# Performance work log

Hardware: AMD Instinct MI355X
Metric: run time of the kernel (lower is better)

The kernel has to match this reference:

```python
import jax, jax.numpy as jnp
import numpy as np

N, E, G, IN, H, L, C = 20000, 320000, 128, 16, 64, 4, 10
AVG_D_LOG = float(np.log(17.0))  # log(avg_degree + 1)


def setup_inputs() -> dict:
    key = jax.random.key(0)
    ks = jax.random.split(key, 24)
    p = lambda k, shape: jax.random.normal(k, shape, dtype=jnp.float32) * 0.05
    return dict(
        h=jax.random.normal(ks[0], (N, IN), jnp.float32),
        snorm_n=jax.random.uniform(ks[1], (N, 1), jnp.float32, 0.05, 1.0),
        embW=p(ks[2], (IN, H)), embB=p(ks[3], (H,)),
        preW=p(ks[4], (L, 2 * H, H)), preB=p(ks[5], (L, H)),
        postW=p(ks[6], (L, 13 * H, H)), postB=p(ks[7], (L, H)),
        mixW=p(ks[8], (L, H, H)), mixB=p(ks[9], (L, H)),
        r1W=p(ks[10], (H, H // 2)), r1B=p(ks[11], (H // 2,)),
        r2W=p(ks[12], (H // 2, H // 4)), r2B=p(ks[13], (H // 4,)),
        r3W=p(ks[14], (H // 4, C)), r3B=p(ks[15], (C,)),
        src=jax.random.randint(ks[16], (E,), 0, N),
        dst=jax.random.randint(ks[17], (E,), 0, N),
        graph_ids=jnp.sort(jax.random.randint(ks[18], (N,), 0, G)),
    )


def _pna_forward(h, snorm_n, embW, embB, preW, preB, postW, postB, mixW, mixB,
                 r1W, r1B, r2W, r2B, r3W, r3B, src, dst, graph_ids):
    # Degree-based scalers (computed once; graph is fixed across layers)
    deg = jax.ops.segment_sum(jnp.ones((E,), h.dtype), dst, num_segments=N)  # [N]
    degc = jnp.maximum(deg, 1.0)[:, None]
    logd = jnp.log(deg + 1.0)
    amp = (logd / AVG_D_LOG)[:, None]                      # amplification scaler
    att = (AVG_D_LOG / jnp.maximum(logd, 1e-5))[:, None]   # attenuation scaler
    has_nb = (deg > 0.0)[:, None]

    x = h @ embW + embB  # node embedding [N, H]
    for i in range(L):
        x_in = x
        # pretrans: per-edge message from cat(h_src, h_dst)  [E, H]
        m = jnp.concatenate([x[src], x[dst]], axis=-1) @ preW[i] + preB[i]
        # multi-aggregator reduce at dst: mean, max, min, std
        mean = jax.ops.segment_sum(m, dst, num_segments=N) / degc
        msq = jax.ops.segment_sum(m * m, dst, num_segments=N) / degc
        std = jnp.sqrt(jax.nn.relu(msq - mean * mean) + 1e-5)
        mx = jnp.where(has_nb, jax.ops.segment_max(m, dst, num_segments=N), 0.0)
        mn = jnp.where(has_nb, jax.ops.segment_min(m, dst, num_segments=N), 0.0)
        agg = jnp.concatenate([mean, mx, mn, std], axis=-1)  # [N, 4H]
        # degree scalers: identity, amplification, attenuation -> [N, 12H]
        scaled = jnp.concatenate([agg, agg * amp, agg * att], axis=-1)
        # posttrans over cat(scaled_agg, h) -> [N, H]
        y = jnp.concatenate([scaled, x], axis=-1) @ postW[i] + postB[i]
        # tower mixing network (LeakyReLU FC)
        y = jax.nn.leaky_relu(y @ mixW[i] + mixB[i])
        y = y * snorm_n          # graph norm
        x = x_in + y             # residual
    # mean-nodes readout per graph
    gsum = jax.ops.segment_sum(x, graph_ids, num_segments=G)
    cnt = jnp.maximum(jax.ops.segment_sum(jnp.ones((N,), x.dtype), graph_ids, num_segments=G), 1.0)
    hg = gsum / cnt[:, None]
    # MLPReadout: two halving ReLU layers + classifier
    hg = jax.nn.relu(hg @ r1W + r1B)
    hg = jax.nn.relu(hg @ r2W + r2B)
    return hg @ r3W + r3B  # [G, C]


def reference(h, snorm_n, embW, embB, preW, preB, postW, postB, mixW, mixB,
              r1W, r1B, r2W, r2B, r3W, r3B, src, dst, graph_ids):
    return _pna_forward(h, snorm_n, embW, embB, preW, preB, postW, postB,
                        mixW, mixB, r1W, r1B, r2W, r2B, r3W, r3B,
                        src, dst, graph_ids)
```

## Files before the change

kernel.cpp:

```cpp
#include <hip/hip_runtime.h>
#include <math.h>

#define N_ 20000
#define E_ 320000
#define G_ 128
#define IN_ 16
#define H_ 64
#define L_ 4
#define C_ 10
#define AVG_D_LOG 2.8332133440562162f

union F4 { float4 v; float f[4]; };

typedef _Float16 h8 __attribute__((ext_vector_type(8)));
typedef _Float16 h4 __attribute__((ext_vector_type(4)));
typedef float f4x __attribute__((ext_vector_type(4)));
#define MFMA16(a, b, c) __builtin_amdgcn_mfma_f32_16x16x32_f16((a), (b), (c), 0, 0, 0)


__global__ __launch_bounds__(256) void k_setup(
    const float* __restrict__ h, const float* __restrict__ embW, const float* __restrict__ embB,
    float* __restrict__ x,
    const float* __restrict__ preW, const float* __restrict__ postW, const float* __restrict__ mixW,
    _Float16* __restrict__ preWT, _Float16* __restrict__ postWT, _Float16* __restrict__ mixWT,
    const int* __restrict__ dst, int* __restrict__ deg) {
  __shared__ float tl[64][68];
  int bb = blockIdx.x, tid = threadIdx.x;
  if (bb < 5000) {
    int n = bb * 4 + (tid >> 6);
    int c = tid & 63;
    float acc = embB[c];
#pragma unroll
    for (int k = 0; k < IN_; k++) acc += h[n * IN_ + k] * embW[k * H_ + c];
    x[n * H_ + c] = acc;
  } else if (bb < 5052) {
    int t = bb - 5000;
    int l = t / 13, kt = t % 13, k0 = kt * 64;
    const float* Wsrc = postW + (size_t)l * 53248;
    _Float16* Wdst = postWT + (size_t)l * 53248;
    int r = tid >> 4, q4 = (tid & 15) * 4;
#pragma unroll
    for (int p = 0; p < 4; p++) {
      int rr = p * 16 + r;
      float4 v = *(const float4*)(Wsrc + (size_t)(k0 + rr) * 64 + q4);
      tl[rr][q4 + 0] = v.x; tl[rr][q4 + 1] = v.y;
      tl[rr][q4 + 2] = v.z; tl[rr][q4 + 3] = v.w;
    }
    __syncthreads();
#pragma unroll
    for (int p = 0; p < 4; p++) {
      int o = p * 256 + tid;
      int c = o >> 4, j4 = (o & 15) * 4;
      h4 hv;
      hv[0] = (_Float16)tl[j4 + 0][c]; hv[1] = (_Float16)tl[j4 + 1][c];
      hv[2] = (_Float16)tl[j4 + 2][c]; hv[3] = (_Float16)tl[j4 + 3][c];
      *(h4*)(Wdst + (size_t)c * 832 + k0 + j4) = hv;
    }
  } else if (bb < 5244) {
    int idx = (bb - 5052) * 256 + tid;
    if (idx < 32768) {
      int l = idx >> 13, r = idx & 8191;
      int c = r >> 6, k = r & 63;
      preWT[idx] = (_Float16)preW[l * 8192 + k * 64 + c];
    } else {
      int j = idx - 32768;
      int l = j >> 12, r = j & 4095;
      int c = r >> 6, k = r & 63;
      mixWT[j] = (_Float16)mixW[l * 4096 + k * 64 + c];
    }
  } else {
    int e = (bb - 5244) * 256 + tid;
    if (e < E_) atomicAdd(&deg[dst[e]], 1);
  }
}


__global__ __launch_bounds__(1024) void k_scan(
    const int* __restrict__ deg, int* __restrict__ offs,
    float* __restrict__ ampv, float* __restrict__ attv,
    float* __restrict__ invd, float* __restrict__ hnb,
    const float* __restrict__ x, const _Float16* __restrict__ preWT,
    const float* __restrict__ preB, _Float16* __restrict__ ah, float* __restrict__ b) {
  int bx = blockIdx.x, tid = threadIdx.x;
  if (bx == 0) {
    __shared__ int sh[1024];
    int t = tid;
    int base = t * 20;
    int local[20];
    int s = 0;
    if (t < 1000) {
#pragma unroll
      for (int c = 0; c < 5; c++) {
        int4 v = *(const int4*)(deg + base + c * 4);
        local[c * 4 + 0] = s; s += v.x;
        local[c * 4 + 1] = s; s += v.y;
        local[c * 4 + 2] = s; s += v.z;
        local[c * 4 + 3] = s; s += v.w;
      }
    }
    sh[t] = s;
    __syncthreads();
    for (int off = 1; off < 1024; off <<= 1) {
      int v = (t >= off) ? sh[t - off] : 0;
      __syncthreads();
      sh[t] += v;
      __syncthreads();
    }
    if (t < 1000) {
      int excl = sh[t] - s;
#pragma unroll
      for (int c = 0; c < 5; c++) {
        int4 o;
        o.x = excl + local[c * 4 + 0];
        o.y = excl + local[c * 4 + 1];
        o.z = excl + local[c * 4 + 2];
        o.w = excl + local[c * 4 + 3];
        *(int4*)(offs + base + c * 4) = o;
      }
    }
    if (t == 0) offs[N_] = sh[1023];
  } else if (bx < 21) {
    int idx = (bx - 1) * 1024 + tid;
    if (idx < N_) {
      float d = (float)deg[idx];
      float logd = logf(d + 1.f);
      ampv[idx] = logd / AVG_D_LOG;
      attv[idx] = AVG_D_LOG / fmaxf(logd, 1e-5f);
      invd[idx] = 1.f / fmaxf(d, 1.f);
      hnb[idx] = d > 0.f ? 1.f : 0.f;
    }
  } else {
    int sub = tid >> 8;
    int t2 = tid & 255;
    int n0 = (bx - 21) * 128 + sub * 32;
    if (n0 >= N_) return;
    int lane = t2 & 63, wv = t2 >> 6;
    int mt = wv & 1, nh = wv >> 1;
    int l15 = lane & 15, k0q = (lane >> 4) * 8;
    int mrow = n0 + mt * 16 + l15;
    const float* xr = x + (size_t)mrow * 64;
    const _Float16* wb0 = preWT + (size_t)(nh * 64 + l15) * 64 + k0q;
    f4x acc0 = {0.f,0.f,0.f,0.f}, acc1 = {0.f,0.f,0.f,0.f}, acc2 = {0.f,0.f,0.f,0.f}, acc3 = {0.f,0.f,0.f,0.f};
#pragma unroll
    for (int kb = 0; kb < 64; kb += 32) {
      int ko = kb + k0q;
      F4 xa, xb2;
      xa.v = *(const float4*)(xr + ko);
      xb2.v = *(const float4*)(xr + ko + 4);
      h8 af;
      af[0]=(_Float16)xa.f[0]; af[1]=(_Float16)xa.f[1]; af[2]=(_Float16)xa.f[2]; af[3]=(_Float16)xa.f[3];
      af[4]=(_Float16)xb2.f[0]; af[5]=(_Float16)xb2.f[1]; af[6]=(_Float16)xb2.f[2]; af[7]=(_Float16)xb2.f[3];
      acc0 = MFMA16(af, *(const h8*)(wb0 + kb), acc0);
      acc1 = MFMA16(af, *(const h8*)(wb0 + 1024 + kb), acc1);
      acc2 = MFMA16(af, *(const h8*)(wb0 + 2048 + kb), acc2);
      acc3 = MFMA16(af, *(const h8*)(wb0 + 3072 + kb), acc3);
    }
    int rbase = n0 + mt * 16 + (lane >> 4) * 4;
    f4x accs[4] = {acc0, acc1, acc2, acc3};
#pragma unroll
    for (int t = 0; t < 4; t++) {
      int col = nh * 64 + t * 16 + l15;
#pragma unroll
      for (int r = 0; r < 4; r++) {
        int n = rbase + r;
        if (col < 64) ah[(size_t)n * 64 + col] = (_Float16)accs[t][r];
        else          b[(size_t)n * 64 + (col - 64)] = accs[t][r] + preB[col - 64];
      }
    }
  }
}


__global__ __launch_bounds__(256) void k_scatter(
    const int* __restrict__ src, const int* __restrict__ dst,
    const int* __restrict__ offs, int* __restrict__ cursor, int* __restrict__ csr) {
  int e = blockIdx.x * 256 + threadIdx.x;
  if (e < E_) {
    int d = dst[e];
    int pos = offs[d] + atomicAdd(&cursor[d], 1);
    csr[pos] = src[e];
  }
}


__global__ __launch_bounds__(256, 5) void k_layer(
    const _Float16* __restrict__ ahin, const float* __restrict__ bin,
    const int* __restrict__ offs, const int* __restrict__ csr,
    const float* __restrict__ invd, const float* __restrict__ hnb,
    const _Float16* __restrict__ WT, const float* __restrict__ Bv,
    const _Float16* __restrict__ mixWT, const float* __restrict__ mixB,
    const float* __restrict__ ampv, const float* __restrict__ attv,
    const float* __restrict__ snorm, float* __restrict__ x,
    const _Float16* __restrict__ preWT, const float* __restrict__ preB,
    _Float16* __restrict__ ahout, float* __restrict__ bout, int do_pre) {
  __shared__ _Float16 aggs[16 * 280];
  __shared__ _Float16 ys[16 * 88];
  __shared__ _Float16 xs[16 * 88];
  __shared__ _Float16 xt[16 * 88];
  __shared__ float xs32[16 * 68];
  __shared__ int csr_s[1024];
  __shared__ int soffs[17];
  __shared__ float scal[48];
  int tid = threadIdx.x;
  int n0 = blockIdx.x * 16;
  int lane = tid & 63, wv = tid >> 6;

  int e0 = offs[n0];
  int ecnt = offs[n0 + 16] - e0;
  {
    int row = tid >> 4, qq = tid & 15;
    F4 xv; xv.v = *(const float4*)(x + (size_t)(n0 + row) * 64 + qq * 4);
    h4 xh;
    xh[0] = (_Float16)xv.f[0]; xh[1] = (_Float16)xv.f[1];
    xh[2] = (_Float16)xv.f[2]; xh[3] = (_Float16)xv.f[3];
    *(h4*)(xt + row * 88 + qq * 4) = xh;
    *(float4*)(xs32 + row * 68 + qq * 4) = xv.v;
  }
  if (tid < 17) soffs[tid] = offs[n0 + tid];
  if (tid >= 32 && tid < 48) {
    int i = tid - 32;
    scal[i] = ampv[n0 + i];
    scal[16 + i] = attv[n0 + i];
    scal[32 + i] = snorm[n0 + i];
  }
  int nlA = tid >> 4, qA = tid & 15;
  F4 bv; bv.v = *(const float4*)(bin + (size_t)(n0 + nlA) * 64 + qA * 4);
  float inv = invd[n0 + nlA], hn = hnb[n0 + nlA];
  int col0 = wv * 16 + (tid & 15);
  float b0v = Bv[col0];
  float mb0 = mixB[col0];
  {
    int cnt = ecnt < 1024 ? ecnt : 1024;
    for (int i = tid; i < cnt; i += 256) csr_s[i] = csr[e0 + i];
  }
  __syncthreads();

  {
    int nl = nlA, q = qA;
    int o0 = soffs[nl];
    int deg = soffs[nl + 1] - o0;
    float sum[4], sq[4], mx[4], mn[4];
#pragma unroll
    for (int i = 0; i < 4; i++) {
      sum[i] = 0.f; sq[i] = 0.f;
      mx[i] = -__builtin_inff(); mn[i] = __builtin_inff();
    }
#define GLD_(S) (*(const h4*)(ahin + (size_t)(S) * 64 + q * 4))
#define PROC1_(AV)                                                       \
    do {                                                                 \
      _Pragma("unroll")                                                  \
      for (int i = 0; i < 4; i++) {                                      \
        float v0 = (float)AV[i];                                         \
        sum[i] += v0; sq[i] += v0 * v0;                                  \
        mx[i] = fmaxf(mx[i], v0); mn[i] = fminf(mn[i], v0);              \
      }                                                                  \
    } while (0)
    if (ecnt <= 1024) {
      int lo = o0 - e0;
      int j = 0;
      h4 A0, A1, A2, A3;
      if (j + 3 < deg) {
        A0 = GLD_(csr_s[lo]);     A1 = GLD_(csr_s[lo + 1]);
        A2 = GLD_(csr_s[lo + 2]); A3 = GLD_(csr_s[lo + 3]);
      }
      for (; j + 7 < deg; j += 4) {
        int s0 = csr_s[lo + j + 4], s1 = csr_s[lo + j + 5];
        int s2 = csr_s[lo + j + 6], s3 = csr_s[lo + j + 7];
        h4 B0 = GLD_(s0), B1 = GLD_(s1), B2 = GLD_(s2), B3 = GLD_(s3);
        PROC1_(A0); PROC1_(A1); PROC1_(A2); PROC1_(A3);
        A0 = B0; A1 = B1; A2 = B2; A3 = B3;
      }
      if (j + 3 < deg) { PROC1_(A0); PROC1_(A1); PROC1_(A2); PROC1_(A3); j += 4; }
      for (; j < deg; j++) { h4 a0 = GLD_(csr_s[lo + j]); PROC1_(a0); }
    } else {
      int j = 0;
      for (; j < deg; j++) { h4 a0 = GLD_(csr[o0 + j]); PROC1_(a0); }
    }
#undef GLD_
#undef PROC1_
    h4 hm, hx, hmn, hs;
#pragma unroll
    for (int i = 0; i < 4; i++) {
      float mean_a = sum[i] * inv;
      float var = sq[i] * inv - mean_a * mean_a;
      hs[i] = (_Float16)sqrtf(fmaxf(var, 0.f) + 1e-5f);
      bool nb = hn > 0.5f;
      hm[i] = (_Float16)(nb ? (mean_a + bv.f[i]) : 0.f);
      hx[i] = (_Float16)(nb ? (mx[i] + bv.f[i]) : 0.f);
      hmn[i] = (_Float16)(nb ? (mn[i] + bv.f[i]) : 0.f);
    }
    _Float16* ap = aggs + nl * 280 + q * 4;
    *(h4*)(ap) = hm;
    *(h4*)(ap + 64) = hx;
    *(h4*)(ap + 128) = hmn;
    *(h4*)(ap + 192) = hs;
  }
  __syncthreads();

  int l15 = lane & 15, k0q = (lane >> 4) * 8;
  const _Float16* ag = aggs + (size_t)l15 * 280 + k0q;
  const _Float16* w0 = WT + (size_t)col0 * 832 + k0q;
  f4x aI = {0.f,0.f,0.f,0.f}, aA = {0.f,0.f,0.f,0.f}, aT = {0.f,0.f,0.f,0.f};
#pragma unroll 4
  for (int kb = 0; kb < 256; kb += 32) {
    h8 af = *(const h8*)(ag + kb);
    aI = MFMA16(af, *(const h8*)(w0 + kb), aI);
    aA = MFMA16(af, *(const h8*)(w0 + 256 + kb), aA);
    aT = MFMA16(af, *(const h8*)(w0 + 512 + kb), aT);
  }
  const _Float16* xtr = xt + (size_t)l15 * 88 + k0q;
#pragma unroll
  for (int kb = 0; kb < 64; kb += 32) {
    h8 af = *(const h8*)(xtr + kb);
    aI = MFMA16(af, *(const h8*)(w0 + 768 + kb), aI);
  }
  int qr = (lane >> 4) * 4;
  int rbase = n0 + qr;
#pragma unroll
  for (int r = 0; r < 4; r++) {
    float amp = scal[qr + r], att = scal[16 + qr + r];
    ys[(qr + r) * 88 + col0] = (_Float16)(aI[r] + b0v + amp * aA[r] + att * aT[r]);
  }
  __syncthreads();
  f4x m0 = {0.f,0.f,0.f,0.f};
  const _Float16* yr = ys + (size_t)l15 * 88 + k0q;
  const _Float16* mw0 = mixWT + (size_t)col0 * 64 + k0q;
#pragma unroll
  for (int kb = 0; kb < 64; kb += 32) {
    h8 af = *(const h8*)(yr + kb);
    m0 = MFMA16(af, *(const h8*)(mw0 + kb), m0);
  }
#pragma unroll
  for (int r = 0; r < 4; r++) {
    int n = rbase + r;
    float sn = scal[32 + qr + r];
    float t0 = m0[r] + mb0; t0 = t0 > 0.f ? t0 : 0.01f * t0;
    float xo0 = xs32[(qr + r) * 68 + col0] + t0 * sn;
    x[(size_t)n * 64 + col0] = xo0;
    xs[(qr + r) * 88 + col0] = (_Float16)xo0;
  }

  if (do_pre) {
    __syncthreads();
    int ch = wv;
    const _Float16* xf = xs + (size_t)l15 * 88 + k0q;
    const _Float16* wb0 = preWT + (size_t)(ch * 32 + l15) * 64 + k0q;
    f4x p0 = {0.f,0.f,0.f,0.f}, p1 = {0.f,0.f,0.f,0.f};
#pragma unroll
    for (int kb = 0; kb < 64; kb += 32) {
      h8 af = *(const h8*)(xf + kb);
      p0 = MFMA16(af, *(const h8*)(wb0 + kb), p0);
      p1 = MFMA16(af, *(const h8*)(wb0 + 1024 + kb), p1);
    }
    int prb = n0 + (lane >> 4) * 4;
    f4x accs[2] = {p0, p1};
#pragma unroll
    for (int t = 0; t < 2; t++) {
      int col = ch * 32 + t * 16 + l15;
#pragma unroll
      for (int r = 0; r < 4; r++) {
        int n = prb + r;
        if (col < 64) ahout[(size_t)n * 64 + col] = (_Float16)accs[t][r];
        else          bout[(size_t)n * 64 + (col - 64)] = accs[t][r] + preB[col - 64];
      }
    }
  }
}


__device__ inline int lower_bound_gid(const int* __restrict__ gid, int val) {
  int lo = 0, hi = N_;
  while (lo < hi) {
    int mid = (lo + hi) >> 1;
    if (gid[mid] < val) lo = mid + 1; else hi = mid;
  }
  return lo;
}

__global__ __launch_bounds__(512) void k_readout_fused(
    const float* __restrict__ x, const int* __restrict__ gid,
    const float* __restrict__ r1W, const float* __restrict__ r1B,
    const float* __restrict__ r2W, const float* __restrict__ r2B,
    const float* __restrict__ r3W, const float* __restrict__ r3B,
    float* __restrict__ out) {
  __shared__ float part[8 * 64];
  __shared__ float hg[64];
  __shared__ float t1[32];
  __shared__ float t2[16];
  int g = blockIdx.x, tid = threadIdx.x;
  int lo = lower_bound_gid(gid, g);
  int hi = lower_bound_gid(gid, g + 1);
  int c = tid & 63, w = tid >> 6;
  float s = 0.f;
  for (int n = lo + w; n < hi; n += 8) s += x[(size_t)n * 64 + c];
  part[w * 64 + c] = s;
  __syncthreads();
  if (w == 0) {
    float tot = 0.f;
#pragma unroll
    for (int p = 0; p < 8; p++) tot += part[p * 64 + c];
    float cnt = (float)(hi - lo);
    if (cnt < 1.f) cnt = 1.f;
    hg[c] = tot / cnt;
  }
  __syncthreads();
  if (tid < 32) {
    float acc = r1B[tid];
#pragma unroll 8
    for (int k = 0; k < 64; k++) acc += hg[k] * r1W[k * 32 + tid];
    t1[tid] = fmaxf(acc, 0.f);
  }
  __syncthreads();
  if (tid < 16) {
    float acc = r2B[tid];
#pragma unroll 8
    for (int k = 0; k < 32; k++) acc += t1[k] * r2W[k * 16 + tid];
    t2[tid] = fmaxf(acc, 0.f);
  }
  __syncthreads();
  if (tid < 10) {
    float acc = r3B[tid];
#pragma unroll
    for (int k = 0; k < 16; k++) acc += t2[k] * r3W[k * 10 + tid];
    out[g * 10 + tid] = acc;
  }
}


extern "C" void kernel_launch(void* const* d_in, const int* in_sizes, int n_in,
                              void* d_out, int out_size, void* d_ws, size_t ws_size,
                              hipStream_t stream) {
  const float* h     = (const float*)d_in[0];
  const float* snorm = (const float*)d_in[1];
  const float* embW  = (const float*)d_in[2];
  const float* embB  = (const float*)d_in[3];
  const float* preW  = (const float*)d_in[4];
  const float* preB  = (const float*)d_in[5];
  const float* postW = (const float*)d_in[6];
  const float* postB = (const float*)d_in[7];
  const float* mixW  = (const float*)d_in[8];
  const float* mixB  = (const float*)d_in[9];
  const float* r1W   = (const float*)d_in[10];
  const float* r1B   = (const float*)d_in[11];
  const float* r2W   = (const float*)d_in[12];
  const float* r2B   = (const float*)d_in[13];
  const float* r3W   = (const float*)d_in[14];
  const float* r3B   = (const float*)d_in[15];
  const int* src     = (const int*)d_in[16];
  const int* dst     = (const int*)d_in[17];
  const int* gid     = (const int*)d_in[18];
  float* out = (float*)d_out;

  char* w = (char*)d_ws;
  float* x        = (float*)w; w += (size_t)N_ * 64 * 4;
  _Float16* ah0   = (_Float16*)w; w += (size_t)N_ * 64 * 2;
  _Float16* ah1   = (_Float16*)w; w += (size_t)N_ * 64 * 2;
  float* b0       = (float*)w; w += (size_t)N_ * 64 * 4;
  float* b1       = (float*)w; w += (size_t)N_ * 64 * 4;
  _Float16* preWT = (_Float16*)w; w += (size_t)4 * 128 * 64 * 2;
  _Float16* postWT= (_Float16*)w; w += (size_t)4 * 64 * 832 * 2;
  _Float16* mixWT = (_Float16*)w; w += (size_t)4 * 64 * 64 * 2;
  float* ampv = (float*)w; w += (size_t)N_ * 4;
  float* attv = (float*)w; w += (size_t)N_ * 4;
  float* invd = (float*)w; w += (size_t)N_ * 4;
  float* hnb  = (float*)w; w += (size_t)N_ * 4;
  int* csr    = (int*)w;   w += (size_t)E_ * 4;
  int* offs   = (int*)w;   w += (size_t)(N_ + 64) * 4;
  int* zbase  = (int*)w;
  int* deg    = (int*)w;   w += (size_t)N_ * 4;
  int* cursor = (int*)w;   w += (size_t)N_ * 4;

  hipMemsetAsync(zbase, 0, (size_t)2 * N_ * 4, stream);
  k_setup<<<6494, 256, 0, stream>>>(h, embW, embB, x, preW, postW, mixW,
                                    preWT, postWT, mixWT, dst, deg);
  k_scan<<<178, 1024, 0, stream>>>(deg, offs, ampv, attv, invd, hnb,
                                   x, preWT, preB, ah0, b0);
  k_scatter<<<1250, 256, 0, stream>>>(src, dst, offs, cursor, csr);
  int gb = N_ / 16;
  _Float16* ahs[2] = {ah0, ah1};
  float* bs[2] = {b0, b1};
  for (int l = 0; l < L_; l++) {
    int pin = l & 1, pout = 1 - pin;
    k_layer<<<gb, 256, 0, stream>>>(ahs[pin], bs[pin], offs, csr, invd, hnb,
                                    postWT + (size_t)l * 53248, postB + l * H_,
                                    mixWT + (size_t)l * 4096, mixB + l * H_,
                                    ampv, attv, snorm, x,
                                    preWT + (size_t)(l + 1 < L_ ? l + 1 : 0) * 8192,
                                    preB + (l + 1 < L_ ? l + 1 : 0) * H_,
                                    ahs[pout], bs[pout], l + 1 < L_ ? 1 : 0);
  }
  k_readout_fused<<<G_, 512, 0, stream>>>(x, gid, r1W, r1B, r2W, r2B, r3W, r3B, out);
}
```

Baseline: 268.7 us.

## Fuse per-layer launches into a persistent kernel with a grid barrier

Measured after the change: 911.2 us. 3.39x slower.

```diff
diff --git a/kernel.cpp b/kernel.cpp
--- a/kernel.cpp
+++ b/kernel.cpp
@@ -8,6 +8,7 @@
 #define H_ 64
 #define L_ 4
 #define C_ 10
+#define GB_ (N_ / 16)
 #define AVG_D_LOG 2.8332133440562162f
 
 union F4 { float4 v; float f[4]; };
@@ -183,38 +184,63 @@
 }
 
 
-__global__ __launch_bounds__(256, 5) void k_layer(
-    const _Float16* __restrict__ ahin, const float* __restrict__ bin,
+__device__ __forceinline__ void grid_bar(int* bar, int tid) {
+  __syncthreads();
+  if (tid == 0) {
+    __threadfence();
+    __hip_atomic_fetch_add(bar, 1, __ATOMIC_RELEASE, __HIP_MEMORY_SCOPE_AGENT);
+    long cnt = 0;
+    int v;
+    do {
+      v = __hip_atomic_load(bar, __ATOMIC_ACQUIRE, __HIP_MEMORY_SCOPE_AGENT);
+      if (v >= GB_) break;
+      __builtin_amdgcn_s_sleep(8);
+    } while (++cnt < (1L << 28));
+    __threadfence();
+  }
+  __syncthreads();
+}
+
+
+__global__ __launch_bounds__(256, 5) void k_layers(
+    const float* __restrict__ bin,
     const int* __restrict__ offs, const int* __restrict__ csr,
     const float* __restrict__ invd, const float* __restrict__ hnb,
-    const _Float16* __restrict__ WT, const float* __restrict__ Bv,
+    const _Float16* __restrict__ postWT, const float* __restrict__ postB,
     const _Float16* __restrict__ mixWT, const float* __restrict__ mixB,
     const float* __restrict__ ampv, const float* __restrict__ attv,
     const float* __restrict__ snorm, float* __restrict__ x,
     const _Float16* __restrict__ preWT, const float* __restrict__ preB,
-    _Float16* __restrict__ ahout, float* __restrict__ bout, int do_pre) {
+    _Float16* __restrict__ ah0g, _Float16* __restrict__ ah1g,
+    int* __restrict__ bar) {
   __shared__ _Float16 aggs[16 * 280];
   __shared__ _Float16 ys[16 * 88];
-  __shared__ _Float16 xs[16 * 88];
-  __shared__ _Float16 xt[16 * 88];
+  __shared__ _Float16 xtA[16 * 88];
+  __shared__ _Float16 xtB[16 * 88];
   __shared__ float xs32[16 * 68];
+  __shared__ float b_lds[16 * 68];
   __shared__ int csr_s[1024];
   __shared__ int soffs[17];
   __shared__ float scal[48];
   int tid = threadIdx.x;
   int n0 = blockIdx.x * 16;
   int lane = tid & 63, wv = tid >> 6;
+  int nlA = tid >> 4, qA = tid & 15;
+  int l15 = lane & 15, k0q = (lane >> 4) * 8;
+  int col0 = wv * 16 + l15;
+  int qr = (lane >> 4) * 4;
 
   int e0 = offs[n0];
   int ecnt = offs[n0 + 16] - e0;
   {
-    int row = tid >> 4, qq = tid & 15;
+    int row = nlA, qq = qA;
     F4 xv; xv.v = *(const float4*)(x + (size_t)(n0 + row) * 64 + qq * 4);
     h4 xh;
     xh[0] = (_Float16)xv.f[0]; xh[1] = (_Float16)xv.f[1];
     xh[2] = (_Float16)xv.f[2]; xh[3] = (_Float16)xv.f[3];
-    *(h4*)(xt + row * 88 + qq * 4) = xh;
+    *(h4*)(xtA + row * 88 + qq * 4) = xh;
     *(float4*)(xs32 + row * 68 + qq * 4) = xv.v;
+    *(float4*)(b_lds + row * 68 + qq * 4) = *(const float4*)(bin + (size_t)(n0 + row) * 64 + qq * 4);
   }
   if (tid < 17) soffs[tid] = offs[n0 + tid];
   if (tid >= 32 && tid < 48) {
@@ -223,146 +249,154 @@
     scal[16 + i] = attv[n0 + i];
     scal[32 + i] = snorm[n0 + i];
   }
-  int nlA = tid >> 4, qA = tid & 15;
-  F4 bv; bv.v = *(const float4*)(bin + (size_t)(n0 + nlA) * 64 + qA * 4);
   float inv = invd[n0 + nlA], hn = hnb[n0 + nlA];
-  int col0 = wv * 16 + (tid & 15);
-  float b0v = Bv[col0];
-  float mb0 = mixB[col0];
   {
     int cnt = ecnt < 1024 ? ecnt : 1024;
     for (int i = tid; i < cnt; i += 256) csr_s[i] = csr[e0 + i];
   }
   __syncthreads();
 
-  {
-    int nl = nlA, q = qA;
-    int o0 = soffs[nl];
-    int deg = soffs[nl + 1] - o0;
-    float sum[4], sq[4], mx[4], mn[4];
-#pragma unroll
-    for (int i = 0; i < 4; i++) {
-      sum[i] = 0.f; sq[i] = 0.f;
-      mx[i] = -__builtin_inff(); mn[i] = __builtin_inff();
-    }
-#define GLD_(S) (*(const h4*)(ahin + (size_t)(S) * 64 + q * 4))
+  for (int l = 0; l < L_; l++) {
+    const _Float16* ahin = (l & 1) ? ah1g : ah0g;
+    _Float16* ahout = (l & 1) ? ah0g : ah1g;
+    const _Float16* WT = postWT + (size_t)l * 53248;
+    const float* Bv = postB + l * H_;
+    const _Float16* mw = mixWT + (size_t)l * 4096;
+    const float* mB = mixB + l * H_;
+    _Float16* xt_cur = (l & 1) ? xtB : xtA;
+    _Float16* xt_nxt = (l & 1) ? xtA : xtB;
+
+    {
+      int o0 = soffs[nlA];
+      int deg = soffs[nlA + 1] - o0;
+      F4 bv; bv.v = *(const float4*)(b_lds + nlA * 68 + qA * 4);
+      float sum[4], sq[4], mx[4], mn[4];
+#pragma unroll
+      for (int i = 0; i < 4; i++) {
+        sum[i] = 0.f; sq[i] = 0.f;
+        mx[i] = -__builtin_inff(); mn[i] = __builtin_inff();
+      }
+#define GLD_(S) (*(const h4*)(ahin + (size_t)(S) * 64 + qA * 4))
 #define PROC1_(AV)                                                       \
-    do {                                                                 \
-      _Pragma("unroll")                                                  \
-      for (int i = 0; i < 4; i++) {                                      \
-        float v0 = (float)AV[i];                                         \
-        sum[i] += v0; sq[i] += v0 * v0;                                  \
-        mx[i] = fmaxf(mx[i], v0); mn[i] = fminf(mn[i], v0);              \
-      }                                                                  \
-    } while (0)
-    if (ecnt <= 1024) {
-      int lo = o0 - e0;
-      int j = 0;
-      h4 A0, A1, A2, A3;
-      if (j + 3 < deg) {
-        A0 = GLD_(csr_s[lo]);     A1 = GLD_(csr_s[lo + 1]);
-        A2 = GLD_(csr_s[lo + 2]); A3 = GLD_(csr_s[lo + 3]);
-      }
-      for (; j + 7 < deg; j += 4) {
-        int s0 = csr_s[lo + j + 4], s1 = csr_s[lo + j + 5];
-        int s2 = csr_s[lo + j + 6], s3 = csr_s[lo + j + 7];
-        h4 B0 = GLD_(s0), B1 = GLD_(s1), B2 = GLD_(s2), B3 = GLD_(s3);
-        PROC1_(A0); PROC1_(A1); PROC1_(A2); PROC1_(A3);
-        A0 = B0; A1 = B1; A2 = B2; A3 = B3;
-      }
-      if (j + 3 < deg) { PROC1_(A0); PROC1_(A1); PROC1_(A2); PROC1_(A3); j += 4; }
-      for (; j < deg; j++) { h4 a0 = GLD_(csr_s[lo + j]); PROC1_(a0); }
-    } else {
-      int j = 0;
-      for (; j < deg; j++) { h4 a0 = GLD_(csr[o0 + j]); PROC1_(a0); }
-    }
+      do {                                                               \
+        _Pragma("unroll")                                                \
+        for (int i = 0; i < 4; i++) {                                    \
+          float v0 = (float)AV[i];                                       \
+          sum[i] += v0; sq[i] += v0 * v0;                                \
+          mx[i] = fmaxf(mx[i], v0); mn[i] = fminf(mn[i], v0);            \
+        }                                                                \
+      } while (0)
+      if (ecnt <= 1024) {
+        int lo = o0 - e0;
+        int j = 0;
+        h4 A0, A1, A2, A3;
+        if (j + 3 < deg) {
+          A0 = GLD_(csr_s[lo]);     A1 = GLD_(csr_s[lo + 1]);
+          A2 = GLD_(csr_s[lo + 2]); A3 = GLD_(csr_s[lo + 3]);
+        }
+        for (; j + 7 < deg; j += 4) {
+          int s0 = csr_s[lo + j + 4], s1 = csr_s[lo + j + 5];
+          int s2 = csr_s[lo + j + 6], s3 = csr_s[lo + j + 7];
+          h4 B0 = GLD_(s0), B1 = GLD_(s1), B2 = GLD_(s2), B3 = GLD_(s3);
+          PROC1_(A0); PROC1_(A1); PROC1_(A2); PROC1_(A3);
+          A0 = B0; A1 = B1; A2 = B2; A3 = B3;
+        }
+        if (j + 3 < deg) { PROC1_(A0); PROC1_(A1); PROC1_(A2); PROC1_(A3); j += 4; }
+        for (; j < deg; j++) { h4 a0 = GLD_(csr_s[lo + j]); PROC1_(a0); }
+      } else {
+        for (int j = 0; j < deg; j++) { h4 a0 = GLD_(csr[o0 + j]); PROC1_(a0); }
+      }
 #undef GLD_
 #undef PROC1_
-    h4 hm, hx, hmn, hs;
-#pragma unroll
-    for (int i = 0; i < 4; i++) {
-      float mean_a = sum[i] * inv;
-      float var = sq[i] * inv - mean_a * mean_a;
-      hs[i] = (_Float16)sqrtf(fmaxf(var, 0.f) + 1e-5f);
-      bool nb = hn > 0.5f;
-      hm[i] = (_Float16)(nb ? (mean_a + bv.f[i]) : 0.f);
-      hx[i] = (_Float16)(nb ? (mx[i] + bv.f[i]) : 0.f);
-      hmn[i] = (_Float16)(nb ? (mn[i] + bv.f[i]) : 0.f);
-    }
-    _Float16* ap = aggs + nl * 280 + q * 4;
-    *(h4*)(ap) = hm;
-    *(h4*)(ap + 64) = hx;
-    *(h4*)(ap + 128) = hmn;
-    *(h4*)(ap + 192) = hs;
-  }
-  __syncthreads();
-
-  int l15 = lane & 15, k0q = (lane >> 4) * 8;
-  const _Float16* ag = aggs + (size_t)l15 * 280 + k0q;
-  const _Float16* w0 = WT + (size_t)col0 * 832 + k0q;
-  f4x aI = {0.f,0.f,0.f,0.f}, aA = {0.f,0.f,0.f,0.f}, aT = {0.f,0.f,0.f,0.f};
+      h4 hm, hx, hmn, hs;
+#pragma unroll
+      for (int i = 0; i < 4; i++) {
+        float mean_a = sum[i] * inv;
+        float var = sq[i] * inv - mean_a * mean_a;
+        hs[i] = (_Float16)sqrtf(fmaxf(var, 0.f) + 1e-5f);
+        bool nb = hn > 0.5f;
+        hm[i] = (_Float16)(nb ? (mean_a + bv.f[i]) : 0.f);
+        hx[i] = (_Float16)(nb ? (mx[i] + bv.f[i]) : 0.f);
+        hmn[i] = (_Float16)(nb ? (mn[i] + bv.f[i]) : 0.f);
+      }
+      _Float16* ap = aggs + nlA * 280 + qA * 4;
+      *(h4*)(ap) = hm;
+      *(h4*)(ap + 64) = hx;
+      *(h4*)(ap + 128) = hmn;
+      *(h4*)(ap + 192) = hs;
+    }
+    __syncthreads();
+
+    {
+      const _Float16* ag = aggs + (size_t)l15 * 280 + k0q;
+      const _Float16* w0 = WT + (size_t)col0 * 832 + k0q;
+      float b0v = Bv[col0];
+      float mb0 = mB[col0];
+      f4x aI = {0.f,0.f,0.f,0.f}, aA = {0.f,0.f,0.f,0.f}, aT = {0.f,0.f,0.f,0.f};
 #pragma unroll 4
-  for (int kb = 0; kb < 256; kb += 32) {
-    h8 af = *(const h8*)(ag + kb);
-    aI = MFMA16(af, *(const h8*)(w0 + kb), aI);
-    aA = MFMA16(af, *(const h8*)(w0 + 256 + kb), aA);
-    aT = MFMA16(af, *(const h8*)(w0 + 512 + kb), aT);
-  }
-  const _Float16* xtr = xt + (size_t)l15 * 88 + k0q;
-#pragma unroll
-  for (int kb = 0; kb < 64; kb += 32) {
-    h8 af = *(const h8*)(xtr + kb);
-    aI = MFMA16(af, *(const h8*)(w0 + 768 + kb), aI);
-  }
-  int qr = (lane >> 4) * 4;
-  int rbase = n0 + qr;
-#pragma unroll
-  for (int r = 0; r < 4; r++) {
-    float amp = scal[qr + r], att = scal[16 + qr + r];
-    ys[(qr + r) * 88 + col0] = (_Float16)(aI[r] + b0v + amp * aA[r] + att * aT[r]);
-  }
-  __syncthreads();
-  f4x m0 = {0.f,0.f,0.f,0.f};
-  const _Float16* yr = ys + (size_t)l15 * 88 + k0q;
-  const _Float16* mw0 = mixWT + (size_t)col0 * 64 + k0q;
-#pragma unroll
-  for (int kb = 0; kb < 64; kb += 32) {
-    h8 af = *(const h8*)(yr + kb);
-    m0 = MFMA16(af, *(const h8*)(mw0 + kb), m0);
-  }
-#pragma unroll
-  for (int r = 0; r < 4; r++) {
-    int n = rbase + r;
-    float sn = scal[32 + qr + r];
-    float t0 = m0[r] + mb0; t0 = t0 > 0.f ? t0 : 0.01f * t0;
-    float xo0 = xs32[(qr + r) * 68 + col0] + t0 * sn;
-    x[(size_t)n * 64 + col0] = xo0;
-    xs[(qr + r) * 88 + col0] = (_Float16)xo0;
-  }
-
-  if (do_pre) {
-    __syncthreads();
-    int ch = wv;
-    const _Float16* xf = xs + (size_t)l15 * 88 + k0q;
-    const _Float16* wb0 = preWT + (size_t)(ch * 32 + l15) * 64 + k0q;
-    f4x p0 = {0.f,0.f,0.f,0.f}, p1 = {0.f,0.f,0.f,0.f};
-#pragma unroll
-    for (int kb = 0; kb < 64; kb += 32) {
-      h8 af = *(const h8*)(xf + kb);
-      p0 = MFMA16(af, *(const h8*)(wb0 + kb), p0);
-      p1 = MFMA16(af, *(const h8*)(wb0 + 1024 + kb), p1);
-    }
-    int prb = n0 + (lane >> 4) * 4;
-    f4x accs[2] = {p0, p1};
-#pragma unroll
-    for (int t = 0; t < 2; t++) {
-      int col = ch * 32 + t * 16 + l15;
+      for (int kb = 0; kb < 256; kb += 32) {
+        h8 af = *(const h8*)(ag + kb);
+        aI = MFMA16(af, *(const h8*)(w0 + kb), aI);
+        aA = MFMA16(af, *(const h8*)(w0 + 256 + kb), aA);
+        aT = MFMA16(af, *(const h8*)(w0 + 512 + kb), aT);
+      }
+      const _Float16* xtr = xt_cur + (size_t)l15 * 88 + k0q;
+#pragma unroll
+      for (int kb = 0; kb < 64; kb += 32) {
+        h8 af = *(const h8*)(xtr + kb);
+        aI = MFMA16(af, *(const h8*)(w0 + 768 + kb), aI);
+      }
 #pragma unroll
       for (int r = 0; r < 4; r++) {
-        int n = prb + r;
-        if (col < 64) ahout[(size_t)n * 64 + col] = (_Float16)accs[t][r];
-        else          bout[(size_t)n * 64 + (col - 64)] = accs[t][r] + preB[col - 64];
-      }
+        float amp = scal[qr + r], att = scal[16 + qr + r];
+        ys[(qr + r) * 88 + col0] = (_Float16)(aI[r] + b0v + amp * aA[r] + att * aT[r]);
+      }
+      __syncthreads();
+      f4x m0 = {0.f,0.f,0.f,0.f};
+      const _Float16* yr = ys + (size_t)l15 * 88 + k0q;
+      const _Float16* mw0 = mw + (size_t)col0 * 64 + k0q;
+#pragma unroll
+      for (int kb = 0; kb < 64; kb += 32) {
+        h8 af = *(const h8*)(yr + kb);
+        m0 = MFMA16(af, *(const h8*)(mw0 + kb), m0);
+      }
+#pragma unroll
+      for (int r = 0; r < 4; r++) {
+        float sn = scal[32 + qr + r];
+        float t0 = m0[r] + mb0; t0 = t0 > 0.f ? t0 : 0.01f * t0;
+        int idx = (qr + r) * 68 + col0;
+        float xo0 = xs32[idx] + t0 * sn;
+        xs32[idx] = xo0;
+        xt_nxt[(qr + r) * 88 + col0] = (_Float16)xo0;
+        if (l == L_ - 1) x[(size_t)(n0 + qr + r) * 64 + col0] = xo0;
+      }
+    }
+
+    if (l < L_ - 1) {
+      __syncthreads();
+      {
+        const _Float16* xf = xt_nxt + (size_t)l15 * 88 + k0q;
+        const _Float16* wb0 = preWT + (size_t)(l + 1) * 8192 + (size_t)(wv * 32 + l15) * 64 + k0q;
+        const float* pB = preB + (l + 1) * H_;
+        f4x p0 = {0.f,0.f,0.f,0.f}, p1 = {0.f,0.f,0.f,0.f};
+#pragma unroll
+        for (int kb = 0; kb < 64; kb += 32) {
+          h8 af = *(const h8*)(xf + kb);
+          p0 = MFMA16(af, *(const h8*)(wb0 + kb), p0);
+          p1 = MFMA16(af, *(const h8*)(wb0 + 1024 + kb), p1);
+        }
+        f4x accs[2] = {p0, p1};
+#pragma unroll
+        for (int t = 0; t < 2; t++) {
+          int col = wv * 32 + t * 16 + l15;
+#pragma unroll
+          for (int r = 0; r < 4; r++) {
+            if (col < 64) ahout[(size_t)(n0 + qr + r) * 64 + col] = (_Float16)accs[t][r];
+            else          b_lds[(qr + r) * 68 + (col - 64)] = accs[t][r] + pB[col - 64];
+          }
+        }
+      }
+      grid_bar(bar + l, tid);
     }
   }
 }
@@ -456,7 +490,6 @@
   _Float16* ah0   = (_Float16*)w; w += (size_t)N_ * 64 * 2;
   _Float16* ah1   = (_Float16*)w; w += (size_t)N_ * 64 * 2;
   float* b0       = (float*)w; w += (size_t)N_ * 64 * 4;
-  float* b1       = (float*)w; w += (size_t)N_ * 64 * 4;
   _Float16* preWT = (_Float16*)w; w += (size_t)4 * 128 * 64 * 2;
   _Float16* postWT= (_Float16*)w; w += (size_t)4 * 64 * 832 * 2;
   _Float16* mixWT = (_Float16*)w; w += (size_t)4 * 64 * 64 * 2;
@@ -469,25 +502,17 @@
   int* zbase  = (int*)w;
   int* deg    = (int*)w;   w += (size_t)N_ * 4;
   int* cursor = (int*)w;   w += (size_t)N_ * 4;
-
-  hipMemsetAsync(zbase, 0, (size_t)2 * N_ * 4, stream);
+  int* bar    = (int*)w;   w += 64;
+
+  hipMemsetAsync(zbase, 0, (size_t)2 * N_ * 4 + 64, stream);
   k_setup<<<6494, 256, 0, stream>>>(h, embW, embB, x, preW, postW, mixW,
                                     preWT, postWT, mixWT, dst, deg);
   k_scan<<<178, 1024, 0, stream>>>(deg, offs, ampv, attv, invd, hnb,
                                    x, preWT, preB, ah0, b0);
   k_scatter<<<1250, 256, 0, stream>>>(src, dst, offs, cursor, csr);
-  int gb = N_ / 16;
-  _Float16* ahs[2] = {ah0, ah1};
-  float* bs[2] = {b0, b1};
-  for (int l = 0; l < L_; l++) {
-    int pin = l & 1, pout = 1 - pin;
-    k_layer<<<gb, 256, 0, stream>>>(ahs[pin], bs[pin], offs, csr, invd, hnb,
-                                    postWT + (size_t)l * 53248, postB + l * H_,
-                                    mixWT + (size_t)l * 4096, mixB + l * H_,
+  k_layers<<<GB_, 256, 0, stream>>>(b0, offs, csr, invd, hnb,
+                                    postWT, postB, mixWT, mixB,
                                     ampv, attv, snorm, x,
-                                    preWT + (size_t)(l + 1 < L_ ? l + 1 : 0) * 8192,
-                                    preB + (l + 1 < L_ ? l + 1 : 0) * H_,
-                                    ahs[pout], bs[pout], l + 1 < L_ ? 1 : 0);
-  }
+                                    preWT, preB, ah0, ah1, bar);
   k_readout_fused<<<G_, 512, 0, stream>>>(x, gid, r1W, r1B, r2W, r2B, r3W, r3B, out);
 }
```
